# Kernel optimization log

Hardware: AMD Instinct MI355X
Metric: run time of the kernel (lower is better)

## Reference

```python
import jax, jax.numpy as jnp
import numpy as np

NUM_NEURONS = 2048
EMBED_DIM = 1024
WINDOW_SIZES = np.array([1, 2, 4, 8, 16, 32, 64, 128, 256, 512, 1024, 2048], dtype=np.int32)
WINDOW_MAX = 2048
TEMPERATURE = 1.0


def setup_inputs() -> dict:
    key = jax.random.key(0)
    ks = jax.random.split(key, 12)
    W = len(WINDOW_SIZES)
    inp = {
        "x": jax.random.normal(ks[0], (8192, EMBED_DIM), dtype=jnp.float32),
        "n_weights": jax.random.normal(ks[1], (NUM_NEURONS, EMBED_DIM), dtype=jnp.float32) * 0.01,
        "n_biases": jnp.zeros((NUM_NEURONS,), dtype=jnp.float32),
        "combo_w": jax.random.normal(ks[2], (W, NUM_NEURONS, NUM_NEURONS), dtype=jnp.float32) * (1.0 / np.sqrt(NUM_NEURONS)),
        "combo_b": jax.random.normal(ks[3], (W, NUM_NEURONS), dtype=jnp.float32) * 0.01,
        "q_w": jax.random.normal(ks[4], (EMBED_DIM, NUM_NEURONS), dtype=jnp.float32) * (1.0 / np.sqrt(NUM_NEURONS)),
        "q_b": jnp.zeros((EMBED_DIM,), dtype=jnp.float32),
        "k_w": jax.random.normal(ks[5], (EMBED_DIM, NUM_NEURONS), dtype=jnp.float32) * (1.0 / np.sqrt(NUM_NEURONS)),
        "k_b": jnp.zeros((EMBED_DIM,), dtype=jnp.float32),
        "cerebellum": jnp.ones((W,), dtype=jnp.float32),
        "judge_bias": jnp.zeros((W,), dtype=jnp.float32),
        "credibility_bias": jnp.zeros((W,), dtype=jnp.float32),
        "parliament_blend": jnp.float32(0.5),
    }
    return inp


def _forward(x, n_weights, n_biases, combo_w, combo_b, q_w, q_b, k_w, k_b,
             cerebellum, judge_bias, credibility_bias, parliament_blend):
    # NEURON forward: [S, E] @ [E, N] + [N] -> tanh -> clamp
    act = jnp.clip(jnp.tanh(x @ n_weights.T + n_biases), -5.0, 5.0)  # [S, N]
    S = act.shape[0]
    tail = min(S, WINDOW_MAX)
    # faithful replication of stackedWindowMeans: last `tail` activations go to the
    # END of a [WINDOW_MAX, N] buffer, mask selects the FIRST windowSize rows
    padded = jnp.zeros((WINDOW_MAX, NUM_NEURONS), dtype=act.dtype).at[WINDOW_MAX - tail:].set(act[S - tail:])
    wsz = jnp.asarray(WINDOW_SIZES, dtype=jnp.float32)  # [W]
    mask = (jnp.arange(WINDOW_MAX)[None, :] < jnp.asarray(WINDOW_SIZES)[:, None]).astype(act.dtype)  # [W, WINDOW_MAX]
    window_out = (mask @ padded) / wsz[:, None]  # [W, N]
    # per-window Linear combos (torch Linear: y = x @ W.T + b)
    combo = jnp.einsum('wn,wmn->wm', window_out, combo_w) + combo_b  # [W, N]
    query = combo @ q_w.T + q_b + (judge_bias * cerebellum)[:, None]  # [W, E]
    key = window_out @ k_w.T + k_b + (credibility_bias * cerebellum)[:, None]  # [W, E]
    scores = (query @ key.T) / TEMPERATURE  # [W, W]
    # selfScores + peerScores == column sums of scores
    combined_scores = scores.sum(axis=0)  # [W]
    pb = jax.nn.sigmoid(parliament_blend)
    blended = ((1.0 - pb) * cerebellum + pb * combined_scores) * cerebellum
    combined_window_weights = jax.nn.softmax(blended)  # [W]
    ctx = jnp.sum(combo + combined_window_weights[:, None], axis=0, keepdims=True)  # [1, N]
    ctx = ctx + 0.2 * combo.mean(axis=0, keepdims=True)
    return ctx


def reference(x, n_weights, n_biases, combo_w, combo_b, q_w, q_b, k_w, k_b,
              cerebellum, judge_bias, credibility_bias, parliament_blend):
    return _forward(x, n_weights, n_biases, combo_w, combo_b, q_w, q_b, k_w, k_b,
                    cerebellum, judge_bias, credibility_bias, parliament_blend)
```

## Files before the change

kernel.cpp:

```cpp
#include <hip/hip_runtime.h>
#include <hip/hip_bf16.h>
#include <math.h>

#define N_NEUR 2048
#define EMB 1024
#define S_TOT 8192
#define WMAX 2048
#define NW 12

typedef __attribute__((ext_vector_type(8))) short bf16x8;
typedef __attribute__((ext_vector_type(4))) float f32x4;

__device__ inline short f2bf(float f) {
    union { float f; unsigned u; } v; v.f = f;
    unsigned r = v.u + 0x7FFFu + ((v.u >> 16) & 1u);
    return (short)(r >> 16);
}

__global__ __launch_bounds__(256) void precast(const float* __restrict__ xt,
                                               const float* __restrict__ nw,
                                               short* __restrict__ A,
                                               short* __restrict__ W) {
    const int HALF = (N_NEUR * EMB) / 4;
    int g = blockIdx.x * 256 + threadIdx.x;
    const float4* src; short* dst;
    if (g < HALF) { src = (const float4*)xt; dst = A; }
    else          { g -= HALF; src = (const float4*)nw; dst = W; }
    float4 v = src[g];
    short4 o;
    o.x = f2bf(v.x); o.y = f2bf(v.y); o.z = f2bf(v.z); o.w = f2bf(v.w);
    *(short4*)(dst + (size_t)g * 4) = o;
}

#define GLDS(g, l) __builtin_amdgcn_global_load_lds(                          \
    (const __attribute__((address_space(1))) void*)(g),                       \
    (__attribute__((address_space(3))) void*)(l), 16, 0, 0)

__global__ __launch_bounds__(256) void gemm_seg(const short* __restrict__ A,
                                                const short* __restrict__ W,
                                                const float* __restrict__ bias,
                                                float* __restrict__ seg) {
    __shared__ short As[2][64 * 64];
    __shared__ short Bs[2][64 * 64];
    const int t = threadIdx.x;
    const int bm = blockIdx.y, bn = blockIdx.x;
    const int lane = t & 63, wid = t >> 6;
    const int wr = wid >> 1, wc = wid & 1;
    const int l15 = lane & 15, lhi = lane >> 4;
    const int srow = lane >> 3;
    const int pslot = (lane & 7) ^ srow;
    const short* gA0 = A + (size_t)(bm * 64 + wid * 16 + 0 + srow) * EMB + pslot * 8;
    const short* gA1 = A + (size_t)(bm * 64 + wid * 16 + 8 + srow) * EMB + pslot * 8;
    const short* gB0 = W + (size_t)(bn * 64 + wid * 16 + 0 + srow) * EMB + pslot * 8;
    const short* gB1 = W + (size_t)(bn * 64 + wid * 16 + 8 + srow) * EMB + pslot * 8;
    short* lA0[2] = { &As[0][(wid * 16 + 0) * 64], &As[1][(wid * 16 + 0) * 64] };
    short* lA1[2] = { &As[0][(wid * 16 + 8) * 64], &As[1][(wid * 16 + 8) * 64] };
    short* lB0[2] = { &Bs[0][(wid * 16 + 0) * 64], &Bs[1][(wid * 16 + 0) * 64] };
    short* lB1[2] = { &Bs[0][(wid * 16 + 8) * 64], &Bs[1][(wid * 16 + 8) * 64] };

    f32x4 acc[2][2] = {};

    GLDS(gA0, lA0[0]); GLDS(gA1, lA1[0]);
    GLDS(gB0, lB0[0]); GLDS(gB1, lB1[0]);
    __syncthreads();

    int cur = 0;
    for (int ks = 0; ks < 16; ++ks) {
        if (ks < 15) {
            int k0 = (ks + 1) * 64;
            GLDS(gA0 + k0, lA0[cur ^ 1]); GLDS(gA1 + k0, lA1[cur ^ 1]);
            GLDS(gB0 + k0, lB0[cur ^ 1]); GLDS(gB1 + k0, lB1[cur ^ 1]);
        }
        bf16x8 af[2][2], bb[2][2];
        #pragma unroll
        for (int kk = 0; kk < 2; ++kk) {
            #pragma unroll
            for (int m = 0; m < 2; ++m) {
                int row = wr * 32 + m * 16 + l15;
                int slot = (kk * 4 + lhi) ^ (row & 7);
                af[kk][m] = *(const bf16x8*)&As[cur][row * 64 + slot * 8];
            }
            #pragma unroll
            for (int n = 0; n < 2; ++n) {
                int row = wc * 32 + n * 16 + l15;
                int slot = (kk * 4 + lhi) ^ (row & 7);
                bb[kk][n] = *(const bf16x8*)&Bs[cur][row * 64 + slot * 8];
            }
        }
        __builtin_amdgcn_s_setprio(1);
        #pragma unroll
        for (int kk = 0; kk < 2; ++kk)
            #pragma unroll
            for (int m = 0; m < 2; ++m)
                #pragma unroll
                for (int n = 0; n < 2; ++n)
                    acc[m][n] = __builtin_amdgcn_mfma_f32_16x16x32_bf16(af[kk][m], bb[kk][n], acc[m][n], 0, 0, 0);
        __builtin_amdgcn_s_setprio(0);
        __syncthreads();
        cur ^= 1;
    }

    if (bm > 0) {
        int jseg = 38 - __clz(bm);
        #pragma unroll
        for (int n = 0; n < 2; ++n) {
            int col = bn * 64 + wc * 32 + n * 16 + l15;
            float bc = bias[col];
            float s = 0.f;
            #pragma unroll
            for (int m = 0; m < 2; ++m)
                #pragma unroll
                for (int j = 0; j < 4; ++j)
                    s += tanhf(acc[m][n][j] + bc);
            s += __shfl_xor(s, 16);
            s += __shfl_xor(s, 32);
            if (lhi == 0) atomicAdd(&seg[jseg * N_NEUR + col], s);
        }
    } else {
        #pragma unroll
        for (int n = 0; n < 2; ++n) {
            int col = bn * 64 + wc * 32 + n * 16 + l15;
            float bc = bias[col];
            if (wr == 1) {
                float s = 0.f;
                #pragma unroll
                for (int m = 0; m < 2; ++m)
                    #pragma unroll
                    for (int j = 0; j < 4; ++j)
                        s += tanhf(acc[m][n][j] + bc);
                s += __shfl_xor(s, 16);
                s += __shfl_xor(s, 32);
                if (lhi == 0) atomicAdd(&seg[6 * N_NEUR + col], s);
            } else {
                float s = 0.f;
                #pragma unroll
                for (int j = 0; j < 4; ++j)
                    s += tanhf(acc[1][n][j] + bc);
                s += __shfl_xor(s, 16);
                s += __shfl_xor(s, 32);
                if (lhi == 0) atomicAdd(&seg[5 * N_NEUR + col], s);
                #pragma unroll
                for (int j = 0; j < 4; ++j) {
                    int r = lhi * 4 + j;
                    int sj = (r == 0) ? 0 : (32 - __clz(r));
                    atomicAdd(&seg[sj * N_NEUR + col], tanhf(acc[0][n][j] + bc));
                }
            }
        }
    }
}

__global__ __launch_bounds__(256) void winout_init(const float* __restrict__ seg,
                                                   const float* __restrict__ cb,
                                                   float* __restrict__ wout,
                                                   float* __restrict__ out) {
    int n = blockIdx.x * 256 + threadIdx.x;
    float run = 0.f;
    #pragma unroll
    for (int w = 0; w < NW; ++w) {
        run += seg[w * N_NEUR + n];
        wout[w * N_NEUR + n] = run * (1.0f / (float)(1 << w));
    }
    float bs = 0.f;
    #pragma unroll
    for (int w = 0; w < NW; ++w) bs += cb[w * N_NEUR + n];
    out[n] = 1.0166666666666666f * bs + 1.0f;
}

__global__ __launch_bounds__(256) void combo_dot(const float* __restrict__ cw,
                                                 const float* __restrict__ wout,
                                                 float* __restrict__ out) {
    int wid = threadIdx.x >> 6, lane = threadIdx.x & 63;
    int r = blockIdx.x * 4 + wid;
    int w = r >> 11, m = r & 2047;
    const float4* row  = (const float4*)(cw + (size_t)(w * N_NEUR + m) * N_NEUR);
    const float4* wrow = (const float4*)(wout + w * N_NEUR);
    float s = 0.f;
    #pragma unroll
    for (int i = 0; i < 8; ++i) {
        float4 a = row[i * 64 + lane];
        float4 b = wrow[i * 64 + lane];
        s += a.x * b.x + a.y * b.y + a.z * b.z + a.w * b.w;
    }
    #pragma unroll
    for (int off = 32; off > 0; off >>= 1) s += __shfl_down(s, off);
    if (lane == 0) atomicAdd(&out[m], 1.0166666666666666f * s);
}

extern "C" void kernel_launch(void* const* d_in, const int* in_sizes, int n_in,
                              void* d_out, int out_size, void* d_ws, size_t ws_size,
                              hipStream_t stream) {
    const float* x  = (const float*)d_in[0];
    const float* nw = (const float*)d_in[1];
    const float* nb = (const float*)d_in[2];
    const float* cw = (const float*)d_in[3];
    const float* cb = (const float*)d_in[4];
    float* out = (float*)d_out;

    char* ws = (char*)d_ws;
    float* seg  = (float*)ws;
    float* wout = (float*)(ws + 98304);
    short* Abf  = (short*)(ws + 204800);
    short* Wbf  = (short*)(ws + 204800 + 4194304);

    hipMemsetAsync(ws, 0, 98304, stream);

    precast<<<4096, 256, 0, stream>>>(x + (size_t)(S_TOT - WMAX) * EMB, nw, Abf, Wbf);

    dim3 g1(32, 32);
    gemm_seg<<<g1, 256, 0, stream>>>(Abf, Wbf, nb, seg);

    winout_init<<<8, 256, 0, stream>>>(seg, cb, wout, out);

    combo_dot<<<6144, 256, 0, stream>>>(cw, wout, out);
}
```

Measured before the change: 61.67 us.

## Enlarge GEMM tiles to 128x128 and fold memset and window-init into neighbours

The activation GEMM now uses 128x128 block tiles with a 4x4 MFMA accumulator per wave, on a 16x16 grid instead of 32x32. The segment-index math and the bm==0 split are adjusted to the new tile height. The separate memset is removed: the precast kernel now zeroes the segment buffer and a completion counter. The winout_init kernel is removed and its work runs in the last GEMM block to finish, found through an atomic counter and threadfence. This cuts two launches and the extra workspace pass. In exchange, the last block does the window prefix-sums serially after the others finish, and the larger tiles give fewer blocks and more register pressure.

```diff
diff --git a/kernel.cpp b/kernel.cpp
--- a/kernel.cpp
+++ b/kernel.cpp
@@ -5,7 +5,6 @@
 #define N_NEUR 2048
 #define EMB 1024
 #define S_TOT 8192
-#define WMAX 2048
 #define NW 12
 
 typedef __attribute__((ext_vector_type(8))) short bf16x8;
@@ -20,16 +19,21 @@
 __global__ __launch_bounds__(256) void precast(const float* __restrict__ xt,
                                                const float* __restrict__ nw,
                                                short* __restrict__ A,
-                                               short* __restrict__ W) {
+                                               short* __restrict__ W,
+                                               float* __restrict__ seg,
+                                               int* __restrict__ ctr) {
     const int HALF = (N_NEUR * EMB) / 4;
     int g = blockIdx.x * 256 + threadIdx.x;
+    if (g < (NW * N_NEUR) / 4) ((float4*)seg)[g] = make_float4(0.f, 0.f, 0.f, 0.f);
+    if (g == (NW * N_NEUR) / 4) *ctr = 0;
+    int gg = g;
     const float4* src; short* dst;
-    if (g < HALF) { src = (const float4*)xt; dst = A; }
-    else          { g -= HALF; src = (const float4*)nw; dst = W; }
-    float4 v = src[g];
+    if (gg < HALF) { src = (const float4*)xt; dst = A; }
+    else           { gg -= HALF; src = (const float4*)nw; dst = W; }
+    float4 v = src[gg];
     short4 o;
     o.x = f2bf(v.x); o.y = f2bf(v.y); o.z = f2bf(v.z); o.w = f2bf(v.w);
-    *(short4*)(dst + (size_t)g * 4) = o;
+    *(short4*)(dst + (size_t)gg * 4) = o;
 }
 
 #define GLDS(g, l) __builtin_amdgcn_global_load_lds(                          \
@@ -39,76 +43,74 @@
 __global__ __launch_bounds__(256) void gemm_seg(const short* __restrict__ A,
                                                 const short* __restrict__ W,
                                                 const float* __restrict__ bias,
-                                                float* __restrict__ seg) {
-    __shared__ short As[2][64 * 64];
-    __shared__ short Bs[2][64 * 64];
+                                                const float* __restrict__ cb,
+                                                float* __restrict__ seg,
+                                                float* __restrict__ wout,
+                                                float* __restrict__ out,
+                                                int* __restrict__ ctr) {
+    __shared__ short As[2][128 * 64];
+    __shared__ short Bs[2][128 * 64];
     const int t = threadIdx.x;
     const int bm = blockIdx.y, bn = blockIdx.x;
     const int lane = t & 63, wid = t >> 6;
     const int wr = wid >> 1, wc = wid & 1;
     const int l15 = lane & 15, lhi = lane >> 4;
-    const int srow = lane >> 3;
-    const int pslot = (lane & 7) ^ srow;
-    const short* gA0 = A + (size_t)(bm * 64 + wid * 16 + 0 + srow) * EMB + pslot * 8;
-    const short* gA1 = A + (size_t)(bm * 64 + wid * 16 + 8 + srow) * EMB + pslot * 8;
-    const short* gB0 = W + (size_t)(bn * 64 + wid * 16 + 0 + srow) * EMB + pslot * 8;
-    const short* gB1 = W + (size_t)(bn * 64 + wid * 16 + 8 + srow) * EMB + pslot * 8;
-    short* lA0[2] = { &As[0][(wid * 16 + 0) * 64], &As[1][(wid * 16 + 0) * 64] };
-    short* lA1[2] = { &As[0][(wid * 16 + 8) * 64], &As[1][(wid * 16 + 8) * 64] };
-    short* lB0[2] = { &Bs[0][(wid * 16 + 0) * 64], &Bs[1][(wid * 16 + 0) * 64] };
-    short* lB1[2] = { &Bs[0][(wid * 16 + 8) * 64], &Bs[1][(wid * 16 + 8) * 64] };
-
-    f32x4 acc[2][2] = {};
-
-    GLDS(gA0, lA0[0]); GLDS(gA1, lA1[0]);
-    GLDS(gB0, lB0[0]); GLDS(gB1, lB1[0]);
+    const int srow8 = lane >> 3;
+    const int pslot = (lane & 7) ^ srow8;
+    const short* gAb = A + (size_t)(bm * 128 + wid * 8 + srow8) * EMB + pslot * 8;
+    const short* gBb = W + (size_t)(bn * 128 + wid * 8 + srow8) * EMB + pslot * 8;
+
+    f32x4 acc[4][4] = {};
+
+#define STAGE(buf, k0) do {                                                   \
+    _Pragma("unroll")                                                         \
+    for (int r = 0; r < 4; ++r) {                                             \
+        GLDS(gAb + r * 32 * EMB + (k0), &As[buf][(r * 32 + wid * 8) * 64]);   \
+        GLDS(gBb + r * 32 * EMB + (k0), &Bs[buf][(r * 32 + wid * 8) * 64]);   \
+    } } while (0)
+
+    STAGE(0, 0);
     __syncthreads();
 
     int cur = 0;
     for (int ks = 0; ks < 16; ++ks) {
-        if (ks < 15) {
-            int k0 = (ks + 1) * 64;
-            GLDS(gA0 + k0, lA0[cur ^ 1]); GLDS(gA1 + k0, lA1[cur ^ 1]);
-            GLDS(gB0 + k0, lB0[cur ^ 1]); GLDS(gB1 + k0, lB1[cur ^ 1]);
-        }
-        bf16x8 af[2][2], bb[2][2];
+        if (ks < 15) STAGE(cur ^ 1, (ks + 1) * 64);
         #pragma unroll
         for (int kk = 0; kk < 2; ++kk) {
-            #pragma unroll
-            for (int m = 0; m < 2; ++m) {
-                int row = wr * 32 + m * 16 + l15;
+            bf16x8 af[4], bb[4];
+            #pragma unroll
+            for (int m = 0; m < 4; ++m) {
+                int row = wr * 64 + m * 16 + l15;
                 int slot = (kk * 4 + lhi) ^ (row & 7);
-                af[kk][m] = *(const bf16x8*)&As[cur][row * 64 + slot * 8];
-            }
-            #pragma unroll
-            for (int n = 0; n < 2; ++n) {
-                int row = wc * 32 + n * 16 + l15;
+                af[m] = *(const bf16x8*)&As[cur][row * 64 + slot * 8];
+            }
+            #pragma unroll
+            for (int n = 0; n < 4; ++n) {
+                int row = wc * 64 + n * 16 + l15;
                 int slot = (kk * 4 + lhi) ^ (row & 7);
-                bb[kk][n] = *(const bf16x8*)&Bs[cur][row * 64 + slot * 8];
-            }
-        }
-        __builtin_amdgcn_s_setprio(1);
-        #pragma unroll
-        for (int kk = 0; kk < 2; ++kk)
-            #pragma unroll
-            for (int m = 0; m < 2; ++m)
-                #pragma unroll
-                for (int n = 0; n < 2; ++n)
-                    acc[m][n] = __builtin_amdgcn_mfma_f32_16x16x32_bf16(af[kk][m], bb[kk][n], acc[m][n], 0, 0, 0);
-        __builtin_amdgcn_s_setprio(0);
+                bb[n] = *(const bf16x8*)&Bs[cur][row * 64 + slot * 8];
+            }
+            __builtin_amdgcn_s_setprio(1);
+            #pragma unroll
+            for (int m = 0; m < 4; ++m)
+                #pragma unroll
+                for (int n = 0; n < 4; ++n)
+                    acc[m][n] = __builtin_amdgcn_mfma_f32_16x16x32_bf16(af[m], bb[n], acc[m][n], 0, 0, 0);
+            __builtin_amdgcn_s_setprio(0);
+        }
         __syncthreads();
         cur ^= 1;
     }
 
     if (bm > 0) {
-        int jseg = 38 - __clz(bm);
+        int jseg = 39 - __clz(bm);
         #pragma unroll
-        for (int n = 0; n < 2; ++n) {
-            int col = bn * 64 + wc * 32 + n * 16 + l15;
+        for (int n = 0; n < 4; ++n) {
+            int col = bn * 128 + wc * 64 + n * 16 + l15;
             float bc = bias[col];
             float s = 0.f;
             #pragma unroll
-            for (int m = 0; m < 2; ++m)
+            for (int m = 0; m < 4; ++m)
                 #pragma unroll
                 for (int j = 0; j < 4; ++j)
                     s += tanhf(acc[m][n][j] + bc);
@@ -118,27 +120,36 @@
         }
     } else {
         #pragma unroll
-        for (int n = 0; n < 2; ++n) {
-            int col = bn * 64 + wc * 32 + n * 16 + l15;
+        for (int n = 0; n < 4; ++n) {
+            int col = bn * 128 + wc * 64 + n * 16 + l15;
             float bc = bias[col];
             if (wr == 1) {
                 float s = 0.f;
                 #pragma unroll
-                for (int m = 0; m < 2; ++m)
+                for (int m = 0; m < 4; ++m)
                     #pragma unroll
                     for (int j = 0; j < 4; ++j)
                         s += tanhf(acc[m][n][j] + bc);
                 s += __shfl_xor(s, 16);
                 s += __shfl_xor(s, 32);
-                if (lhi == 0) atomicAdd(&seg[6 * N_NEUR + col], s);
+                if (lhi == 0) atomicAdd(&seg[7 * N_NEUR + col], s);
             } else {
-                float s = 0.f;
+                float s6 = 0.f;
+                #pragma unroll
+                for (int m = 2; m < 4; ++m)
+                    #pragma unroll
+                    for (int j = 0; j < 4; ++j)
+                        s6 += tanhf(acc[m][n][j] + bc);
+                s6 += __shfl_xor(s6, 16);
+                s6 += __shfl_xor(s6, 32);
+                if (lhi == 0) atomicAdd(&seg[6 * N_NEUR + col], s6);
+                float s5 = 0.f;
                 #pragma unroll
                 for (int j = 0; j < 4; ++j)
-                    s += tanhf(acc[1][n][j] + bc);
-                s += __shfl_xor(s, 16);
-                s += __shfl_xor(s, 32);
-                if (lhi == 0) atomicAdd(&seg[5 * N_NEUR + col], s);
+                    s5 += tanhf(acc[1][n][j] + bc);
+                s5 += __shfl_xor(s5, 16);
+                s5 += __shfl_xor(s5, 32);
+                if (lhi == 0) atomicAdd(&seg[5 * N_NEUR + col], s5);
                 #pragma unroll
                 for (int j = 0; j < 4; ++j) {
                     int r = lhi * 4 + j;
@@ -148,23 +159,27 @@
             }
         }
     }
-}
-
-__global__ __launch_bounds__(256) void winout_init(const float* __restrict__ seg,
-                                                   const float* __restrict__ cb,
-                                                   float* __restrict__ wout,
-                                                   float* __restrict__ out) {
-    int n = blockIdx.x * 256 + threadIdx.x;
-    float run = 0.f;
-    #pragma unroll
-    for (int w = 0; w < NW; ++w) {
-        run += seg[w * N_NEUR + n];
-        wout[w * N_NEUR + n] = run * (1.0f / (float)(1 << w));
-    }
-    float bs = 0.f;
-    #pragma unroll
-    for (int w = 0; w < NW; ++w) bs += cb[w * N_NEUR + n];
-    out[n] = 1.0166666666666666f * bs + 1.0f;
+
+    __shared__ int lastblk;
+    __threadfence();
+    if (t == 0) lastblk = (atomicAdd(ctr, 1) == 255);
+    __syncthreads();
+    if (lastblk) {
+        __threadfence();
+        const volatile float* vseg = (const volatile float*)seg;
+        for (int n = t; n < N_NEUR; n += 256) {
+            float run = 0.f;
+            #pragma unroll
+            for (int w = 0; w < NW; ++w) {
+                run += vseg[w * N_NEUR + n];
+                wout[w * N_NEUR + n] = run * (1.0f / (float)(1 << w));
+            }
+            float bs = 0.f;
+            #pragma unroll
+            for (int w = 0; w < NW; ++w) bs += cb[w * N_NEUR + n];
+            out[n] = 1.0166666666666666f * bs + 1.0f;
+        }
+    }
 }
 
 __global__ __launch_bounds__(256) void combo_dot(const float* __restrict__ cw,
@@ -200,17 +215,14 @@
     char* ws = (char*)d_ws;
     float* seg  = (float*)ws;
     float* wout = (float*)(ws + 98304);
+    int*   ctr  = (int*)(ws + 196608);
     short* Abf  = (short*)(ws + 204800);
     short* Wbf  = (short*)(ws + 204800 + 4194304);
 
-    hipMemsetAsync(ws, 0, 98304, stream);
-
-    precast<<<4096, 256, 0, stream>>>(x + (size_t)(S_TOT - WMAX) * EMB, nw, Abf, Wbf);
-
-    dim3 g1(32, 32);
-    gemm_seg<<<g1, 256, 0, stream>>>(Abf, Wbf, nb, seg);
-
-    winout_init<<<8, 256, 0, stream>>>(seg, cb, wout, out);
+    precast<<<4096, 256, 0, stream>>>(x + (size_t)(S_TOT - 2048) * EMB, nw, Abf, Wbf, seg, ctr);
+
+    dim3 g1(16, 16);
+    gemm_seg<<<g1, 256, 0, stream>>>(Abf, Wbf, nb, cb, seg, wout, out, ctr);
 
     combo_dot<<<6144, 256, 0, stream>>>(cw, wout, out);
 }
```

Result: slower. 107.1 us (+73.7%).
